# Performance work log

Hardware: AMD Instinct MI355X
Metric: run time of the kernel (lower is better)

## Reference

```python
import jax, jax.numpy as jnp
import numpy as np

META_HIDDEN = 32


def _meta_apply(t, mw1, mb1, mw2, mb2):
    # t: [..., 3] triples; meta MLP 3 -> META_HIDDEN -> 1 (ReLU)
    h = jax.nn.relu(jnp.einsum('...k,hk->...h', t, mw1) + mb1)
    return jnp.einsum('...h,h->...', h, mw2[0]) + mb2[0]


def _meta_update_layer(v_in, w, v_out, mw1, mb1, mw2, mb2):
    # v_in: [I] (batch-0 input activations), w: [O, I], v_out: [O] (batch-0 output activations)
    # Builds the triples [v_i, w_ij, v_j] for every (i, j) pair and runs one batched meta pass.
    t = jnp.stack([
        jnp.broadcast_to(v_in[None, :], w.shape),
        w,
        jnp.broadcast_to(v_out[:, None], w.shape),
    ], axis=-1)  # [O, I, 3]
    return _meta_apply(t, mw1, mb1, mw2, mb2)  # [O, I] new weights


def setup_inputs() -> dict:
    key = jax.random.key(0)
    ks = jax.random.split(key, 12)
    I, H1, H2, O, B = 1024, 2048, 2048, 1024, 32
    def lin(kw, fan_in, fan_out):
        s = 1.0 / np.sqrt(fan_in)
        return jax.random.uniform(kw, (fan_out, fan_in), jnp.float32, -s, s)
    x = jax.random.normal(ks[0], (B, I), jnp.float32)
    w1 = lin(ks[1], I, H1); b1 = jax.random.uniform(ks[2], (H1,), jnp.float32, -1/np.sqrt(I), 1/np.sqrt(I))
    w2 = lin(ks[3], H1, H2); b2 = jax.random.uniform(ks[4], (H2,), jnp.float32, -1/np.sqrt(H1), 1/np.sqrt(H1))
    w3 = lin(ks[5], H2, O); b3 = jax.random.uniform(ks[6], (O,), jnp.float32, -1/np.sqrt(H2), 1/np.sqrt(H2))
    # meta network 3 -> META_HIDDEN -> 1
    mw1 = lin(ks[7], 3, META_HIDDEN); mb1 = jax.random.uniform(ks[8], (META_HIDDEN,), jnp.float32, -1/np.sqrt(3), 1/np.sqrt(3))
    mw2 = lin(ks[9], META_HIDDEN, 1); mb2 = jax.random.uniform(ks[10], (1,), jnp.float32, -1/np.sqrt(META_HIDDEN), 1/np.sqrt(META_HIDDEN))
    return {"x": x, "w1": w1, "b1": b1, "w2": w2, "b2": b2, "w3": w3, "b3": b3,
            "mw1": mw1, "mb1": mb1, "mw2": mw2, "mb2": mb2}


def reference(x, w1, b1, w2, b2, w3, b3, mw1, mb1, mw2, mb2):
    # Main 3-layer MLP forward (ReLU after every layer, including the last, as in the source).
    a0 = x
    a1 = jax.nn.relu(a0 @ w1.T + b1)
    a2 = jax.nn.relu(a1 @ w2.T + b2)
    out = jax.nn.relu(a2 @ w3.T + b3)
    # Per-weight meta update: original code loops over every (input, output) neuron pair of
    # each fc weight and writes meta_weight([v_i, w_ij, v_j]) back into the weight.
    # Only batch row 0 of the activations is used (impulse[i].data[0, idx]).
    nw1 = _meta_update_layer(a0[0], w1, a1[0], mw1, mb1, mw2, mb2)
    nw2 = _meta_update_layer(a1[0], w2, a2[0], mw1, mb1, mw2, mb2)
    nw3 = _meta_update_layer(a2[0], w3, out[0], mw1, mb1, mw2, mb2)
    return out, nw1, nw2, nw3
```

## Files before the change

kernel.cpp:

```cpp
#include <hip/hip_runtime.h>

#define NT 256

typedef unsigned int uint;
typedef unsigned short ushort_t;
typedef float f2 __attribute__((ext_vector_type(2)));
typedef short bh8 __attribute__((ext_vector_type(8)));
typedef float f32x4 __attribute__((ext_vector_type(4)));
typedef uint u32x4 __attribute__((ext_vector_type(4)));

__device__ __forceinline__ void gload16(const float* g, float* l) {
  __builtin_amdgcn_global_load_lds(
      (const __attribute__((address_space(1))) void*)g,
      (__attribute__((address_space(3))) void*)l, 16, 0, 0);
}

__device__ __forceinline__ uint hi2(float a, float b) {
  return (__float_as_uint(a) >> 16) | (__float_as_uint(b) & 0xffff0000u);
}
__device__ __forceinline__ uint lo2(float a, float b) {
  const float r0 = a - __uint_as_float(__float_as_uint(a) & 0xffff0000u);
  const float r1 = b - __uint_as_float(__float_as_uint(b) & 0xffff0000u);
  return hi2(r0, r1);
}
__device__ __forceinline__ void split8v(float4 v0, float4 v1, bh8& hi, bh8& lo) {
  u32x4 h = {hi2(v0.x, v0.y), hi2(v0.z, v0.w), hi2(v1.x, v1.y), hi2(v1.z, v1.w)};
  u32x4 t = {lo2(v0.x, v0.y), lo2(v0.z, v0.w), lo2(v1.x, v1.y), lo2(v1.z, v1.w)};
  hi = __builtin_bit_cast(bh8, h);
  lo = __builtin_bit_cast(bh8, t);
}

__device__ __forceinline__ void meta_body(
    int g,
    const float* __restrict__ w1, const float* __restrict__ w2, const float* __restrict__ w3,
    const float* __restrict__ a0, const float* __restrict__ a1, const float* __restrict__ a2,
    const float* __restrict__ a3,
    float* __restrict__ n1, float* __restrict__ n2, float* __restrict__ n3,
    const float* __restrict__ mw1, const float* __restrict__ mb1,
    const float* __restrict__ mw2, const float* __restrict__ mb2) {
  const int n1c = (2048 * 1024) / 8;
  const int n2c = (2048 * 2048) / 8;

  const float* W; const float* vin; const float* vout; float* nw;
  int sh, e;
  if (g < n1c)            { W = w1; vin = a0; vout = a1; nw = n1; sh = 10; e = g; }
  else if (g < n1c + n2c) { W = w2; vin = a1; vout = a2; nw = n2; sh = 11; e = g - n1c; }
  else                    { W = w3; vin = a2; vout = a3; nw = n3; sh = 11; e = g - n1c - n2c; }

  const int base = e << 3;
  const int o = base >> sh;
  const int i0 = base & ((1 << sh) - 1);

  f2 wv[4], vv[4];
  {
    float4 t0 = *reinterpret_cast<const float4*>(&W[base]);
    float4 t1 = *reinterpret_cast<const float4*>(&W[base + 4]);
    wv[0] = (f2){t0.x, t0.y}; wv[1] = (f2){t0.z, t0.w};
    wv[2] = (f2){t1.x, t1.y}; wv[3] = (f2){t1.z, t1.w};
    float4 u0 = *reinterpret_cast<const float4*>(&vin[i0]);
    float4 u1 = *reinterpret_cast<const float4*>(&vin[i0 + 4]);
    vv[0] = (f2){u0.x, u0.y}; vv[1] = (f2){u0.z, u0.w};
    vv[2] = (f2){u1.x, u1.y}; vv[3] = (f2){u1.z, u1.w};
  }
  const float vo = vout[o];
  const float c2 = mb2[0];

  float r[32];
  #pragma unroll
  for (int j = 0; j < 32; ++j)
    r[j] = fmaf(mw1[3 * j + 2], vo, mb1[j]);

  f2 acc[4];
  #pragma unroll
  for (int p = 0; p < 4; ++p) acc[p] = (f2){c2, c2};

  const f2 zero = (f2){0.f, 0.f};
  #pragma unroll
  for (int j = 0; j < 32; ++j) {
    const float aj = mw1[3 * j];
    const float bj = mw1[3 * j + 1];
    const float mj = mw2[j];
    const f2 a2v = (f2){aj, aj};
    const f2 b2v = (f2){bj, bj};
    const f2 m2v = (f2){mj, mj};
    const f2 r2v = (f2){r[j], r[j]};
    #pragma unroll
    for (int p = 0; p < 4; ++p) {
#if __has_builtin(__builtin_elementwise_fma) && __has_builtin(__builtin_elementwise_max)
      f2 q = __builtin_elementwise_fma(a2v, vv[p], r2v);
      f2 h = __builtin_elementwise_fma(b2v, wv[p], q);
      h = __builtin_elementwise_max(h, zero);
      acc[p] = __builtin_elementwise_fma(m2v, h, acc[p]);
#else
      f2 h;
      h.x = fmaxf(fmaf(bj, wv[p].x, fmaf(aj, vv[p].x, r[j])), 0.f);
      h.y = fmaxf(fmaf(bj, wv[p].y, fmaf(aj, vv[p].y, r[j])), 0.f);
      acc[p].x = fmaf(mj, h.x, acc[p].x);
      acc[p].y = fmaf(mj, h.y, acc[p].y);
#endif
    }
  }

  *reinterpret_cast<float4*>(&nw[base])     = make_float4(acc[0].x, acc[0].y, acc[1].x, acc[1].y);
  *reinterpret_cast<float4*>(&nw[base + 4]) = make_float4(acc[2].x, acc[2].y, acc[3].x, acc[3].y);
}

template<int KL, int OBL, int AF32>
__device__ __forceinline__ void gemm_fwd(
    int gb, int tid,
    const float* __restrict__ Af32, const ushort_t* __restrict__ Ahi,
    const ushort_t* __restrict__ Alo,
    const float* __restrict__ W, int K, int O,
    float* __restrict__ P, float* __restrict__ Wt) {
  const int ob = gb & ((1 << OBL) - 1);
  const int sl = gb >> OBL;
  const int w = tid >> 6, l = tid & 63;
  const int l15 = l & 15, lk = l >> 4;
  const int b0 = (w & 1) << 4;
  const int ow = (w >> 1) << 6;
  const int obase = ob << 7;
  const int kbeg = sl * KL;
  const int bA = b0 + l15;

  f32x4 acc[4];
  #pragma unroll
  for (int of = 0; of < 4; ++of)
    #pragma unroll
    for (int e = 0; e < 4; ++e) acc[of][e] = 0.f;

  #pragma unroll 1
  for (int c = 0; c < KL / 32; ++c) {
    const int kc = kbeg + (c << 5);
    bh8 ahi, alo;
    const int kk = kc + (lk << 3);
    if constexpr (AF32) {
      const float4 v0 = *reinterpret_cast<const float4*>(&Af32[(size_t)bA * K + kk]);
      const float4 v1 = *reinterpret_cast<const float4*>(&Af32[(size_t)bA * K + kk + 4]);
      split8v(v0, v1, ahi, alo);
    } else {
      ahi = *reinterpret_cast<const bh8*>(&Ahi[(size_t)bA * K + kk]);
      alo = *reinterpret_cast<const bh8*>(&Alo[(size_t)bA * K + kk]);
    }
    #pragma unroll
    for (int q = 0; q < 4; ++q) {
      const int s = (q << 8) + tid;
      const int r = s >> 3;
      const int p = s & 7;
      const float* gp = &W[(size_t)(obase + r) * K + kc + ((p ^ (r & 7)) << 2)];
      gload16(gp, Wt + ((s & ~63) << 2));
    }
    __syncthreads();

    #pragma unroll
    for (int of = 0; of < 4; ++of) {
      const int lr = ow + (of << 4) + l15;
      const int cb = lk << 1;
      const float4 w0 = *reinterpret_cast<const float4*>(
          &Wt[(lr << 5) + ((cb ^ (lr & 7)) << 2)]);
      const float4 w1 = *reinterpret_cast<const float4*>(
          &Wt[(lr << 5) + (((cb + 1) ^ (lr & 7)) << 2)]);
      bh8 whi, wlo;
      split8v(w0, w1, whi, wlo);
      acc[of] = __builtin_amdgcn_mfma_f32_16x16x32_bf16(ahi, whi, acc[of], 0, 0, 0);
      acc[of] = __builtin_amdgcn_mfma_f32_16x16x32_bf16(ahi, wlo, acc[of], 0, 0, 0);
      acc[of] = __builtin_amdgcn_mfma_f32_16x16x32_bf16(alo, whi, acc[of], 0, 0, 0);
    }
    __syncthreads();
  }

  #pragma unroll
  for (int of = 0; of < 4; ++of) {
    const int o = obase + ow + (of << 4) + l15;
    #pragma unroll
    for (int r = 0; r < 4; ++r) {
      const int b = b0 + lk * 4 + r;
      P[((size_t)sl * 32 + b) * O + o] = acc[of][r];
    }
  }
}

__device__ __forceinline__ void gemv_body(
    int lbid, int tid,
    const float* __restrict__ vX, const float* __restrict__ vW,
    const float* __restrict__ vB, float* __restrict__ vR, int vK) {
  const int w = tid >> 6, l = tid & 63;
  const int obase = lbid * 16 + w * 4;
  const int nt = vK >> 8;
  float4 xv[8];
  #pragma unroll 8
  for (int t = 0; t < nt; ++t)
    xv[t] = *reinterpret_cast<const float4*>(&vX[(l + (t << 6)) << 2]);
  #pragma unroll
  for (int q = 0; q < 4; ++q) {
    const int o = obase + q;
    const float* wr = vW + (size_t)o * vK;
    float a = 0.f;
    #pragma unroll 8
    for (int t = 0; t < nt; ++t) {
      const float4 wv = *reinterpret_cast<const float4*>(&wr[(l + (t << 6)) << 2]);
      a = fmaf(wv.x, xv[t].x, a); a = fmaf(wv.y, xv[t].y, a);
      a = fmaf(wv.z, xv[t].z, a); a = fmaf(wv.w, xv[t].w, a);
    }
    #pragma unroll
    for (int m = 32; m >= 1; m >>= 1)
      a += __shfl_xor(a, m, 64);
    if (l == 0) vR[o] = fmaxf(a + vB[o], 0.f);
  }
}

template<int MODE, int OSH>
__device__ __forceinline__ void red_body(
    int lbid, int tid, const float* __restrict__ P, const float* __restrict__ bias,
    ushort_t* __restrict__ aHi, ushort_t* __restrict__ aLo,
    float* __restrict__ outF, float* __restrict__ row0) {
  const int idx = lbid * NT + tid;
  const int b = idx >> OSH;
  const int o = idx & ((1 << OSH) - 1);
  float s = 0.f;
  #pragma unroll
  for (int sl = 0; sl < 16; ++sl)
    s += P[(size_t)((sl * 32 + b) << OSH) + o];
  const float v = fmaxf(s + bias[o], 0.f);
  if constexpr (MODE == 0) {
    const uint u = __float_as_uint(v);
    aHi[(size_t)(b << OSH) + o] = (ushort_t)(u >> 16);
    const float hi = __uint_as_float(u & 0xffff0000u);
    aLo[(size_t)(b << OSH) + o] = (ushort_t)(__float_as_uint(v - hi) >> 16);
  } else {
    outF[(size_t)(b << OSH) + o] = v;
  }
  if (row0 != nullptr && b == 0) row0[o] = v;
}

template<int KL, int OBL, int AF32, int RMODE, int ROSH>
__global__ __launch_bounds__(NT) void fused(
    int nGemm, const float* Af32, const ushort_t* Ahi, const ushort_t* Alo,
    const float* W, int K, int O, float* P,
    int nGemv, const float* vX, const float* vW, const float* vB, float* vR, int vK,
    int nRed, const float* RP, const float* Rb, ushort_t* rHi, ushort_t* rLo,
    float* rOut, float* rRow0,
    int mStart,
    const float* w1, const float* w2, const float* w3,
    const float* a0, const float* a1r, const float* a2r, const float* a3r,
    float* n1, float* n2, float* n3,
    const float* mw1, const float* mb1, const float* mw2, const float* mb2) {
  const int bid = blockIdx.x;
  const int tid = threadIdx.x;
  if (bid < nGemm) {
    __shared__ float Wt[128 * 32];
    gemm_fwd<KL, OBL, AF32>(bid, tid, Af32, Ahi, Alo, W, K, O, P, Wt);
    return;
  }
  int b = bid - nGemm;
  if (b < nGemv) { gemv_body(b, tid, vX, vW, vB, vR, vK); return; }
  b -= nGemv;
  if (b < nRed) { red_body<RMODE, ROSH>(b, tid, RP, Rb, rHi, rLo, rOut, rRow0); return; }
  b -= nRed;
  const int g = mStart + b * NT + tid;
  meta_body(g, w1, w2, w3, a0, a1r, a2r, a3r, n1, n2, n3, mw1, mb1, mw2, mb2);
}

extern "C" void kernel_launch(void* const* d_in, const int* in_sizes, int n_in,
                              void* d_out, int out_size, void* d_ws, size_t ws_size,
                              hipStream_t stream) {
  const float* x   = (const float*)d_in[0];
  const float* w1  = (const float*)d_in[1];
  const float* b1  = (const float*)d_in[2];
  const float* w2  = (const float*)d_in[3];
  const float* b2  = (const float*)d_in[4];
  const float* w3  = (const float*)d_in[5];
  const float* b3  = (const float*)d_in[6];
  const float* mw1 = (const float*)d_in[7];
  const float* mb1 = (const float*)d_in[8];
  const float* mw2 = (const float*)d_in[9];
  const float* mb2 = (const float*)d_in[10];

  float* out = (float*)d_out;
  float* n1  = out + 32 * 1024;
  float* n2  = n1 + 2048 * 1024;
  float* n3  = n2 + 2048 * 2048;

  float* ws = (float*)d_ws;
  float* row01  = ws;
  float* row02  = row01 + 2048;
  float* outrow = row02 + 2048;
  ushort_t* a1hi = (ushort_t*)(outrow + 1024);
  ushort_t* a1lo = a1hi + 65536;
  ushort_t* a2hi = a1lo + 65536;
  ushort_t* a2lo = a2hi + 65536;
  float* P1 = (float*)(a2lo + 65536);
  float* P2 = P1 + 1048576;
  float* P3 = P2 + 1048576;

  #define MARGS w1, w2, w3, x, row01, row02, outrow, n1, n2, n3, mw1, mb1, mw2, mb2
  #define NOGEMM 0, (const float*)nullptr, (const ushort_t*)nullptr, (const ushort_t*)nullptr, (const float*)nullptr, 0, 0, (float*)nullptr
  #define NOGEMV 0, (const float*)nullptr, (const float*)nullptr, (const float*)nullptr, (float*)nullptr, 0
  #define NORED  0, (const float*)nullptr, (const float*)nullptr, (ushort_t*)nullptr, (ushort_t*)nullptr, (float*)nullptr, (float*)nullptr

  fused<64, 4, 1, 0, 11><<<256, NT, 0, stream>>>(
      256, x, nullptr, nullptr, w1, 1024, 2048, P1,
      NOGEMV, NORED, 0, MARGS);

  fused<64, 4, 0, 0, 11><<<256, NT, 0, stream>>>(
      NOGEMM, NOGEMV,
      256, P1, b1, a1hi, a1lo, nullptr, row01,
      0, MARGS);

  fused<128, 4, 0, 0, 11><<<1280, NT, 0, stream>>>(
      256, nullptr, a1hi, a1lo, w2, 2048, 2048, P2,
      NOGEMV, NORED, 0, MARGS);

  fused<64, 4, 0, 0, 11><<<256, NT, 0, stream>>>(
      NOGEMM, NOGEMV,
      256, P2, b2, a2hi, a2lo, nullptr, row02,
      0, MARGS);

  fused<128, 3, 0, 0, 11><<<2240, NT, 0, stream>>>(
      128, nullptr, a2hi, a2lo, w3, 2048, 1024, P3,
      64, row02, w3, b3, outrow, 2048,
      NORED, 262144, MARGS);

  fused<64, 4, 0, 1, 10><<<1152, NT, 0, stream>>>(
      NOGEMM, NOGEMV,
      128, P3, b3, nullptr, nullptr, out, nullptr,
      786432, MARGS);

  #undef MARGS
  #undef NOGEMM
  #undef NOGEMV
  #undef NORED
}
```

Before: 53.03 us.

## Compute meta output activations in-block and rebalance meta work across launches

The meta-update blocks now compute the batch-0 output activation themselves. Each block reduces W row segments against the input row with wave shuffles and shared memory, then adds bias and ReLU, so the separate GEMV pass and the outrow buffer go away. This also removes the dependency that forced the layer-3 meta work into the last launch, so meta chunks are redistributed. Layer-1 meta now overlaps the first GEMM, layer-2 meta overlaps the second GEMM, and the final reduction launch shrinks. The cost is an extra __syncthreads and block-level reduction in every meta block, and the code relies on each 256-thread block covering exactly one or two full output rows.

```diff
diff --git a/kernel.cpp b/kernel.cpp
--- a/kernel.cpp
+++ b/kernel.cpp
@@ -33,23 +33,24 @@
 __device__ __forceinline__ void meta_body(
     int g,
     const float* __restrict__ w1, const float* __restrict__ w2, const float* __restrict__ w3,
-    const float* __restrict__ a0, const float* __restrict__ a1, const float* __restrict__ a2,
-    const float* __restrict__ a3,
+    const float* __restrict__ a0, const float* __restrict__ r1, const float* __restrict__ r2,
+    const float* __restrict__ bb1, const float* __restrict__ bb2, const float* __restrict__ bb3,
     float* __restrict__ n1, float* __restrict__ n2, float* __restrict__ n3,
     const float* __restrict__ mw1, const float* __restrict__ mb1,
     const float* __restrict__ mw2, const float* __restrict__ mb2) {
   const int n1c = (2048 * 1024) / 8;
   const int n2c = (2048 * 2048) / 8;
 
-  const float* W; const float* vin; const float* vout; float* nw;
+  const float* W; const float* vin; const float* bias; float* nw;
   int sh, e;
-  if (g < n1c)            { W = w1; vin = a0; vout = a1; nw = n1; sh = 10; e = g; }
-  else if (g < n1c + n2c) { W = w2; vin = a1; vout = a2; nw = n2; sh = 11; e = g - n1c; }
-  else                    { W = w3; vin = a2; vout = a3; nw = n3; sh = 11; e = g - n1c - n2c; }
+  if (g < n1c)            { W = w1; vin = a0; bias = bb1; nw = n1; sh = 10; e = g; }
+  else if (g < n1c + n2c) { W = w2; vin = r1; bias = bb2; nw = n2; sh = 11; e = g - n1c; }
+  else                    { W = w3; vin = r2; bias = bb3; nw = n3; sh = 11; e = g - n1c - n2c; }
 
   const int base = e << 3;
   const int o = base >> sh;
   const int i0 = base & ((1 << sh) - 1);
+  const int tid = threadIdx.x;
 
   f2 wv[4], vv[4];
   {
@@ -62,9 +63,23 @@
     vv[0] = (f2){u0.x, u0.y}; vv[1] = (f2){u0.z, u0.w};
     vv[2] = (f2){u1.x, u1.y}; vv[3] = (f2){u1.z, u1.w};
   }
-  const float vo = vout[o];
+
+  float part = 0.f;
+  #pragma unroll
+  for (int p = 0; p < 4; ++p)
+    part += wv[p].x * vv[p].x + wv[p].y * vv[p].y;
+  #pragma unroll
+  for (int m = 32; m >= 1; m >>= 1)
+    part += __shfl_xor(part, m, 64);
+  __shared__ float msum[4];
+  if ((tid & 63) == 0) msum[tid >> 6] = part;
+  __syncthreads();
+  float vo;
+  if (sh == 10) vo = (tid < 128) ? (msum[0] + msum[1]) : (msum[2] + msum[3]);
+  else          vo = (msum[0] + msum[1]) + (msum[2] + msum[3]);
+  vo = fmaxf(vo + bias[o], 0.f);
+
   const float c2 = mb2[0];
-
   float r[32];
   #pragma unroll
   for (int j = 0; j < 32; ++j)
@@ -179,35 +194,6 @@
   }
 }
 
-__device__ __forceinline__ void gemv_body(
-    int lbid, int tid,
-    const float* __restrict__ vX, const float* __restrict__ vW,
-    const float* __restrict__ vB, float* __restrict__ vR, int vK) {
-  const int w = tid >> 6, l = tid & 63;
-  const int obase = lbid * 16 + w * 4;
-  const int nt = vK >> 8;
-  float4 xv[8];
-  #pragma unroll 8
-  for (int t = 0; t < nt; ++t)
-    xv[t] = *reinterpret_cast<const float4*>(&vX[(l + (t << 6)) << 2]);
-  #pragma unroll
-  for (int q = 0; q < 4; ++q) {
-    const int o = obase + q;
-    const float* wr = vW + (size_t)o * vK;
-    float a = 0.f;
-    #pragma unroll 8
-    for (int t = 0; t < nt; ++t) {
-      const float4 wv = *reinterpret_cast<const float4*>(&wr[(l + (t << 6)) << 2]);
-      a = fmaf(wv.x, xv[t].x, a); a = fmaf(wv.y, xv[t].y, a);
-      a = fmaf(wv.z, xv[t].z, a); a = fmaf(wv.w, xv[t].w, a);
-    }
-    #pragma unroll
-    for (int m = 32; m >= 1; m >>= 1)
-      a += __shfl_xor(a, m, 64);
-    if (l == 0) vR[o] = fmaxf(a + vB[o], 0.f);
-  }
-}
-
 template<int MODE, int OSH>
 __device__ __forceinline__ void red_body(
     int lbid, int tid, const float* __restrict__ P, const float* __restrict__ bias,
@@ -236,12 +222,12 @@
 __global__ __launch_bounds__(NT) void fused(
     int nGemm, const float* Af32, const ushort_t* Ahi, const ushort_t* Alo,
     const float* W, int K, int O, float* P,
-    int nGemv, const float* vX, const float* vW, const float* vB, float* vR, int vK,
     int nRed, const float* RP, const float* Rb, ushort_t* rHi, ushort_t* rLo,
     float* rOut, float* rRow0,
     int mStart,
     const float* w1, const float* w2, const float* w3,
-    const float* a0, const float* a1r, const float* a2r, const float* a3r,
+    const float* a0, const float* r1, const float* r2,
+    const float* bb1, const float* bb2, const float* bb3,
     float* n1, float* n2, float* n3,
     const float* mw1, const float* mb1, const float* mw2, const float* mb2) {
   const int bid = blockIdx.x;
@@ -252,12 +238,11 @@
     return;
   }
   int b = bid - nGemm;
-  if (b < nGemv) { gemv_body(b, tid, vX, vW, vB, vR, vK); return; }
-  b -= nGemv;
   if (b < nRed) { red_body<RMODE, ROSH>(b, tid, RP, Rb, rHi, rLo, rOut, rRow0); return; }
   b -= nRed;
   const int g = mStart + b * NT + tid;
-  meta_body(g, w1, w2, w3, a0, a1r, a2r, a3r, n1, n2, n3, mw1, mb1, mw2, mb2);
+  meta_body(g, w1, w2, w3, a0, r1, r2, bb1, bb2, bb3,
+            n1, n2, n3, mw1, mb1, mw2, mb2);
 }
 
 extern "C" void kernel_launch(void* const* d_in, const int* in_sizes, int n_in,
@@ -283,8 +268,7 @@
   float* ws = (float*)d_ws;
   float* row01  = ws;
   float* row02  = row01 + 2048;
-  float* outrow = row02 + 2048;
-  ushort_t* a1hi = (ushort_t*)(outrow + 1024);
+  ushort_t* a1hi = (ushort_t*)(row02 + 2048);
   ushort_t* a1lo = a1hi + 65536;
   ushort_t* a2hi = a1lo + 65536;
   ushort_t* a2lo = a2hi + 65536;
@@ -292,41 +276,38 @@
   float* P2 = P1 + 1048576;
   float* P3 = P2 + 1048576;
 
-  #define MARGS w1, w2, w3, x, row01, row02, outrow, n1, n2, n3, mw1, mb1, mw2, mb2
+  #define MARGS w1, w2, w3, x, row01, row02, b1, b2, b3, n1, n2, n3, mw1, mb1, mw2, mb2
   #define NOGEMM 0, (const float*)nullptr, (const ushort_t*)nullptr, (const ushort_t*)nullptr, (const float*)nullptr, 0, 0, (float*)nullptr
-  #define NOGEMV 0, (const float*)nullptr, (const float*)nullptr, (const float*)nullptr, (float*)nullptr, 0
   #define NORED  0, (const float*)nullptr, (const float*)nullptr, (ushort_t*)nullptr, (ushort_t*)nullptr, (float*)nullptr, (float*)nullptr
 
-  fused<64, 4, 1, 0, 11><<<256, NT, 0, stream>>>(
+  fused<64, 4, 1, 0, 11><<<1280, NT, 0, stream>>>(
       256, x, nullptr, nullptr, w1, 1024, 2048, P1,
-      NOGEMV, NORED, 0, MARGS);
+      NORED, 0, MARGS);
 
   fused<64, 4, 0, 0, 11><<<256, NT, 0, stream>>>(
-      NOGEMM, NOGEMV,
+      NOGEMM,
       256, P1, b1, a1hi, a1lo, nullptr, row01,
       0, MARGS);
 
-  fused<128, 4, 0, 0, 11><<<1280, NT, 0, stream>>>(
+  fused<128, 4, 0, 0, 11><<<2304, NT, 0, stream>>>(
       256, nullptr, a1hi, a1lo, w2, 2048, 2048, P2,
-      NOGEMV, NORED, 0, MARGS);
+      NORED, 262144, MARGS);
 
   fused<64, 4, 0, 0, 11><<<256, NT, 0, stream>>>(
-      NOGEMM, NOGEMV,
+      NOGEMM,
       256, P2, b2, a2hi, a2lo, nullptr, row02,
       0, MARGS);
 
-  fused<128, 3, 0, 0, 11><<<2240, NT, 0, stream>>>(
+  fused<128, 3, 0, 0, 11><<<1152, NT, 0, stream>>>(
       128, nullptr, a2hi, a2lo, w3, 2048, 1024, P3,
-      64, row02, w3, b3, outrow, 2048,
-      NORED, 262144, MARGS);
-
-  fused<64, 4, 0, 1, 10><<<1152, NT, 0, stream>>>(
-      NOGEMM, NOGEMV,
+      NORED, 786432, MARGS);
+
+  fused<64, 4, 0, 1, 10><<<128, NT, 0, stream>>>(
+      NOGEMM,
       128, P3, b3, nullptr, nullptr, out, nullptr,
-      786432, MARGS);
+      0, MARGS);
 
   #undef MARGS
   #undef NOGEMM
-  #undef NOGEMV
   #undef NORED
 }
```

Result: no change. 52.30 us (-1.4%).
